# Kernel tuning notes

Measured on AMD Instinct MI355X. Metric: run time of the kernel, lower is better.

## Reference

```python
import jax, jax.numpy as jnp
import numpy as np

N_NODES = 1_000_000
N_EDGES = 16_000_000


def setup_inputs() -> dict:
    key = jax.random.key(0)
    ks = jax.random.split(key, 8)
    x = jax.random.normal(ks[0], (N_NODES, 9), dtype=jnp.float32)
    edge_index = jax.random.randint(ks[1], (2, N_EDGES), 0, N_NODES, dtype=jnp.int64)
    # Glorot-ish scaled params
    W1 = jax.random.normal(ks[2], (9, 16), dtype=jnp.float32) * 0.3
    b1 = jax.random.normal(ks[3], (16,), dtype=jnp.float32) * 0.01
    W2 = jax.random.normal(ks[4], (16, 10), dtype=jnp.float32) * 0.25
    b2 = jax.random.normal(ks[5], (10,), dtype=jnp.float32) * 0.01
    Wf = jax.random.normal(ks[6], (10, 1), dtype=jnp.float32) * 0.3
    bf = jax.random.normal(ks[7], (1,), dtype=jnp.float32) * 0.01
    return {"x": x, "edge_index": edge_index, "W1": W1, "b1": b1,
            "W2": W2, "b2": b2, "Wf": Wf, "bf": bf}


def _gcn_conv(x, W, b, row, col, norm, n):
    # PyG GCNConv: linear transform, then normalized scatter-add aggregation.
    h = x @ W                                   # [N, out]
    msg = h[row] * norm[:, None]                # gather + edgewise scale [E+N, out]
    out = jax.ops.segment_sum(msg, col, num_segments=n)  # scatter-add [N, out]
    return out + b


def reference(x, edge_index, W1, b1, W2, b2, Wf, bf):
    n = x.shape[0]
    # add self-loops (PyG default add_self_loops=True)
    loop = jnp.arange(n, dtype=edge_index.dtype)
    row = jnp.concatenate([edge_index[0], loop])
    col = jnp.concatenate([edge_index[1], loop])
    # symmetric normalization: deg computed over target nodes, weight 1 per edge
    deg = jax.ops.segment_sum(jnp.ones(row.shape[0], dtype=x.dtype), col,
                              num_segments=n)
    deg_inv_sqrt = jnp.where(deg > 0, jax.lax.rsqrt(jnp.maximum(deg, 1.0)), 0.0)
    norm = deg_inv_sqrt[row] * deg_inv_sqrt[col]  # [E+N]

    h = _gcn_conv(x, W1, b1, row, col, norm, n)
    h = jax.nn.relu(h)
    # dropout is identity in eval mode
    h = _gcn_conv(h, W2, b2, row, col, norm, n)
    return h @ Wf + bf
```

## Files before the change

kernel.cpp:

```cpp
#include <hip/hip_runtime.h>

static constexpr int NN = 1000000;
static constexpr int NE = 16000000;
static constexpr int BSH = 11;
static constexpr int BNODES = 1 << BSH;
static constexpr int BMASK = BNODES - 1;
static constexpr int NB = (NN + BMASK) >> BSH;
static constexpr int NWG = 512;
static constexpr int EPW = NE / NWG;


__global__ void k_count(const int* __restrict__ col, int* __restrict__ counts) {
    __shared__ int cnt[NB];
    for (int i = threadIdx.x; i < NB; i += blockDim.x) cnt[i] = 0;
    __syncthreads();
    long long e0 = (long long)blockIdx.x * EPW;
    long long e1 = e0 + EPW; if (e1 > NE) e1 = NE;
    long long e = e0 + threadIdx.x;
    for (; e + 768 < e1; e += 1024) {
        int c0 = col[e], c1 = col[e + 256], c2 = col[e + 512], c3 = col[e + 768];
        atomicAdd(&cnt[c0 >> BSH], 1);
        atomicAdd(&cnt[c1 >> BSH], 1);
        atomicAdd(&cnt[c2 >> BSH], 1);
        atomicAdd(&cnt[c3 >> BSH], 1);
    }
    for (; e < e1; e += 256) atomicAdd(&cnt[col[e] >> BSH], 1);
    __syncthreads();
    int w = blockIdx.x;
    for (int i = threadIdx.x; i < NB; i += blockDim.x)
        counts[i * NWG + w] = cnt[i];
}


__global__ void k_scan_wg(int* __restrict__ counts, int* __restrict__ bucketTotal) {
    __shared__ int sm[NWG];
    int b = blockIdx.x, t = threadIdx.x;
    int v = counts[b * NWG + t];
    sm[t] = v;
    __syncthreads();
    for (int off = 1; off < NWG; off <<= 1) {
        int x = (t >= off) ? sm[t - off] : 0;
        __syncthreads();
        sm[t] += x;
        __syncthreads();
    }
    counts[b * NWG + t] = sm[t] - v;
    if (t == NWG - 1) bucketTotal[b] = sm[t];
}


__global__ void k_scan_total(const int* __restrict__ bucketTotal,
                             int* __restrict__ bucketBase, int* __restrict__ ptr) {
    __shared__ int sm[512];
    int t = threadIdx.x;
    int v = (t < NB) ? bucketTotal[t] : 0;
    sm[t] = v;
    __syncthreads();
    for (int off = 1; off < 512; off <<= 1) {
        int x = (t >= off) ? sm[t - off] : 0;
        __syncthreads();
        sm[t] += x;
        __syncthreads();
    }
    if (t < NB) bucketBase[t] = sm[t] - v;
    if (t == 0) { bucketBase[NB] = NE; ptr[NN] = NE; }
}


__global__ void k_bin2(const int* __restrict__ row, const int* __restrict__ col,
                       const int* __restrict__ counts, const int* __restrict__ bucketBase,
                       unsigned* __restrict__ binned) {
    __shared__ int off[NB];
    int w = blockIdx.x;
    for (int i = threadIdx.x; i < NB; i += blockDim.x)
        off[i] = bucketBase[i] + counts[i * NWG + w];
    __syncthreads();
    long long e0 = (long long)w * EPW;
    long long e1 = e0 + EPW; if (e1 > NE) e1 = NE;
    long long e = e0 + threadIdx.x;
    for (; e + 768 < e1; e += 1024) {
        int c0 = col[e],       r0 = row[e];
        int c1 = col[e + 256], r1 = row[e + 256];
        int c2 = col[e + 512], r2 = row[e + 512];
        int c3 = col[e + 768], r3 = row[e + 768];
        int p0 = atomicAdd(&off[c0 >> BSH], 1);
        int p1 = atomicAdd(&off[c1 >> BSH], 1);
        int p2 = atomicAdd(&off[c2 >> BSH], 1);
        int p3 = atomicAdd(&off[c3 >> BSH], 1);
        binned[p0] = ((unsigned)r0 << BSH) | (unsigned)(c0 & BMASK);
        binned[p1] = ((unsigned)r1 << BSH) | (unsigned)(c1 & BMASK);
        binned[p2] = ((unsigned)r2 << BSH) | (unsigned)(c2 & BMASK);
        binned[p3] = ((unsigned)r3 << BSH) | (unsigned)(c3 & BMASK);
    }
    for (; e < e1; e += 256) {
        int c = col[e], r = row[e];
        int p = atomicAdd(&off[c >> BSH], 1);
        binned[p] = ((unsigned)r << BSH) | (unsigned)(c & BMASK);
    }
}


__global__ __launch_bounds__(512) void k_ptr_dis(const unsigned* __restrict__ binned,
                                                 const int* __restrict__ bucketBase,
                                                 int* __restrict__ ptr,
                                                 float* __restrict__ dis) {
    __shared__ int cnt[BNODES];
    __shared__ int tsum[512];
    int b = blockIdx.x, t = threadIdx.x;
    for (int i = t; i < BNODES; i += 512) cnt[i] = 0;
    __syncthreads();
    int i0 = bucketBase[b], i1 = bucketBase[b + 1];
    int i = i0 + t;
    for (; i + 1536 < i1; i += 2048) {
        unsigned v0 = binned[i],        v1 = binned[i + 512];
        unsigned v2 = binned[i + 1024], v3 = binned[i + 1536];
        atomicAdd(&cnt[v0 & BMASK], 1);
        atomicAdd(&cnt[v1 & BMASK], 1);
        atomicAdd(&cnt[v2 & BMASK], 1);
        atomicAdd(&cnt[v3 & BMASK], 1);
    }
    for (; i < i1; i += 512) atomicAdd(&cnt[binned[i] & BMASK], 1);
    __syncthreads();
    int s0 = cnt[t * 4], s1 = cnt[t * 4 + 1], s2 = cnt[t * 4 + 2], s3 = cnt[t * 4 + 3];
    int tot = s0 + s1 + s2 + s3;
    tsum[t] = tot;
    __syncthreads();
    for (int off = 1; off < 512; off <<= 1) {
        int x = (t >= off) ? tsum[t - off] : 0;
        __syncthreads();
        tsum[t] += x;
        __syncthreads();
    }
    int base = bucketBase[b] + tsum[t] - tot;
    int n0 = (b << BSH) + t * 4;
    if (n0 < NN)     { ptr[n0]     = base;               dis[n0]     = rsqrtf((float)(s0 + 1)); }
    if (n0 + 1 < NN) { ptr[n0 + 1] = base + s0;          dis[n0 + 1] = rsqrtf((float)(s1 + 1)); }
    if (n0 + 2 < NN) { ptr[n0 + 2] = base + s0 + s1;     dis[n0 + 2] = rsqrtf((float)(s2 + 1)); }
    if (n0 + 3 < NN) { ptr[n0 + 3] = base + s0 + s1 + s2; dis[n0 + 3] = rsqrtf((float)(s3 + 1)); }
}


__global__ void k_bucket_scatter(const unsigned* __restrict__ binned,
                                 const int* __restrict__ bucketBase,
                                 const int* __restrict__ ptr,
                                 int* __restrict__ sortedRow) {
    __shared__ int cur[BNODES];
    int b = blockIdx.x;
    int nodeBase = b << BSH;
    for (int i = threadIdx.x; i < BNODES; i += blockDim.x) {
        int n = nodeBase + i;
        cur[i] = (n < NN) ? ptr[n] : 0;
    }
    __syncthreads();
    int i0 = bucketBase[b], i1 = bucketBase[b + 1];
    int i = i0 + threadIdx.x;
    for (; i + 768 < i1; i += 1024) {
        unsigned v0 = binned[i],       v1 = binned[i + 256];
        unsigned v2 = binned[i + 512], v3 = binned[i + 768];
        int p0 = atomicAdd(&cur[v0 & BMASK], 1);
        int p1 = atomicAdd(&cur[v1 & BMASK], 1);
        int p2 = atomicAdd(&cur[v2 & BMASK], 1);
        int p3 = atomicAdd(&cur[v3 & BMASK], 1);
        sortedRow[p0] = (int)(v0 >> BSH);
        sortedRow[p1] = (int)(v1 >> BSH);
        sortedRow[p2] = (int)(v2 >> BSH);
        sortedRow[p3] = (int)(v3 >> BSH);
    }
    for (; i < i1; i += 256) {
        unsigned v = binned[i];
        int pos = atomicAdd(&cur[v & BMASK], 1);
        sortedRow[pos] = (int)(v >> BSH);
    }
}


__global__ void k_lin1(const float* __restrict__ x, const float* __restrict__ W1,
                       const float* __restrict__ dis, float* __restrict__ g1) {
    __shared__ float w[144];
    if (threadIdx.x < 144) w[threadIdx.x] = W1[threadIdx.x];
    __syncthreads();
    int i = blockIdx.x * blockDim.x + threadIdx.x;
    if (i >= NN) return;
    float xv[9];
#pragma unroll
    for (int k = 0; k < 9; ++k) xv[k] = x[(long long)i * 9 + k];
    float d = dis[i];
#pragma unroll
    for (int j = 0; j < 16; ++j) {
        float acc = 0.f;
#pragma unroll
        for (int k = 0; k < 9; ++k) acc = fmaf(xv[k], w[k * 16 + j], acc);
        g1[(long long)i * 16 + j] = acc * d;
    }
}


template <int MODE>
__global__ void k_pull_f(const int* __restrict__ ptr, const int* __restrict__ sortedRow,
                         const float* __restrict__ dis, const float* __restrict__ g,
                         const float* __restrict__ p0, const float* __restrict__ p1,
                         const float* __restrict__ p2, float* __restrict__ dst) {
    __shared__ float w2s[256];
    __shared__ float c16[16];
    __shared__ float wf16[16];
    __shared__ float bfs;
    if (MODE == 0) {
        if (threadIdx.x < 256) {
            int k = threadIdx.x >> 4, j = threadIdx.x & 15;
            w2s[threadIdx.x] = (j < 10) ? p1[k * 10 + j] : 0.f;
        }
        if (threadIdx.x < 16) c16[threadIdx.x] = p0[threadIdx.x];
    } else {
        if (threadIdx.x < 16) {
            c16[threadIdx.x]  = (threadIdx.x < 10) ? p0[threadIdx.x] : 0.f;
            wf16[threadIdx.x] = (threadIdx.x < 10) ? p1[threadIdx.x] : 0.f;
        }
        if (threadIdx.x == 0) bfs = p2[0];
    }
    __syncthreads();

    int grp = threadIdx.x >> 4;
    int j = threadIdx.x & 15;
    int n = blockIdx.x * 16 + grp;
    if (n >= NN) return;
    int e0 = ptr[n], e1 = ptr[n + 1];
    float acc = g[(long long)n * 16 + j];
    int e = e0;
    for (; e + 16 <= e1; e += 16) {
        int r[16];
#pragma unroll
        for (int k = 0; k < 16; ++k) r[k] = sortedRow[e + k];
        float v[16];
#pragma unroll
        for (int k = 0; k < 16; ++k) v[k] = g[(long long)r[k] * 16 + j];
        float s0 = ((v[0] + v[1]) + (v[2] + v[3])) + ((v[4] + v[5]) + (v[6] + v[7]));
        float s1 = ((v[8] + v[9]) + (v[10] + v[11])) + ((v[12] + v[13]) + (v[14] + v[15]));
        acc += s0 + s1;
    }
    for (; e + 4 <= e1; e += 4) {
        int r0 = sortedRow[e + 0], r1 = sortedRow[e + 1];
        int r2 = sortedRow[e + 2], r3 = sortedRow[e + 3];
        float v0 = g[(long long)r0 * 16 + j];
        float v1 = g[(long long)r1 * 16 + j];
        float v2 = g[(long long)r2 * 16 + j];
        float v3 = g[(long long)r3 * 16 + j];
        acc += (v0 + v1) + (v2 + v3);
    }
    for (; e < e1; ++e)
        acc += g[(long long)sortedRow[e] * 16 + j];

    float d = dis[n];
    float val = d * acc;
    if (MODE == 0) {
        float hv = fmaxf(val + c16[j], 0.f);
        float o = 0.f;
#pragma unroll
        for (int k = 0; k < 16; ++k)
            o = fmaf(__shfl(hv, k, 16), w2s[k * 16 + j], o);
        dst[(long long)n * 16 + j] = o * d;
    } else {
        float t = (val + c16[j]) * wf16[j];
#pragma unroll
        for (int m = 8; m >= 1; m >>= 1) t += __shfl_xor(t, m, 16);
        if (j == 0) dst[n] = t + bfs;
    }
}

extern "C" void kernel_launch(void* const* d_in, const int* in_sizes, int n_in,
                              void* d_out, int out_size, void* d_ws, size_t ws_size,
                              hipStream_t stream) {
    const float* x  = (const float*)d_in[0];
    const int*   ei = (const int*)d_in[1];
    const float* W1 = (const float*)d_in[2];
    const float* b1 = (const float*)d_in[3];
    const float* W2 = (const float*)d_in[4];
    const float* b2 = (const float*)d_in[5];
    const float* Wf = (const float*)d_in[6];
    const float* bf = (const float*)d_in[7];
    float* out = (float*)d_out;

    const int* row = ei;
    const int* col = ei + NE;

    char* ws = (char*)d_ws;
    size_t off = 0;
    auto alloc = [&](size_t bytes) -> void* {
        void* p = ws + off;
        off += (bytes + 255) & ~255ULL;
        return p;
    };
    int* counts      = (int*)alloc((size_t)NB * NWG * 4);
    int* bucketTotal = (int*)alloc((size_t)NB * 4);
    int* bucketBase  = (int*)alloc((size_t)(NB + 1) * 4);
    int* ptr         = (int*)alloc((size_t)(NN + 1) * 4);
    float* dis       = (float*)alloc((size_t)NN * 4);
    unsigned* binned = (unsigned*)alloc((size_t)NE * 4);
    int* sortedRow   = (int*)alloc((size_t)NE * 4);
    float* g1        = (float*)alloc((size_t)NN * 16 * 4);

    float* g2 = (float*)binned;

    const int TB = 256;
    const int nodeGrid = (NN + TB - 1) / TB;
    const int pullGrid = (NN + 15) / 16;

    k_count<<<NWG, TB, 0, stream>>>(col, counts);
    k_scan_wg<<<NB, NWG, 0, stream>>>(counts, bucketTotal);
    k_scan_total<<<1, 512, 0, stream>>>(bucketTotal, bucketBase, ptr);
    k_bin2<<<NWG, TB, 0, stream>>>(row, col, counts, bucketBase, binned);
    k_ptr_dis<<<NB, 512, 0, stream>>>(binned, bucketBase, ptr, dis);
    k_bucket_scatter<<<NB, TB, 0, stream>>>(binned, bucketBase, ptr, sortedRow);

    k_lin1<<<nodeGrid, TB, 0, stream>>>(x, W1, dis, g1);
    k_pull_f<0><<<pullGrid, TB, 0, stream>>>(ptr, sortedRow, dis, g1, b1, W2, nullptr, g2);
    k_pull_f<1><<<pullGrid, TB, 0, stream>>>(ptr, sortedRow, dis, g2, b2, Wf, bf, out);
}
```

Baseline: 1.060 ms.

## Stage binned edges in LDS for coalesced writes; fuse ptr/dis with bucket scatter

The bucket binning kernel now stages packed edges per bucket in shared memory and flushes them in contiguous 16-element chunks. This replaces scattered single-word global writes with short contiguous runs, and entries that overflow the staging capacity fall back to direct atomic writes. The degree/ptr kernel is fused with the per-bucket scatter, so the binned array is read twice within one launch and the ptr reload is removed. The costs are large shared-memory use (about 47KB per block), extra barriers each tile, and serial per-bucket flush loops.

```diff
diff --git a/kernel.cpp b/kernel.cpp
--- a/kernel.cpp
+++ b/kernel.cpp
@@ -8,6 +8,9 @@
 static constexpr int NB = (NN + BMASK) >> BSH;
 static constexpr int NWG = 512;
 static constexpr int EPW = NE / NWG;
+static constexpr int CHUNK = 16;
+static constexpr int CAP = 24;
+static constexpr int KE = 4;
 
 
 __global__ void k_count(const int* __restrict__ col, int* __restrict__ counts) {
@@ -67,43 +70,74 @@
 }
 
 
-__global__ void k_bin2(const int* __restrict__ row, const int* __restrict__ col,
-                       const int* __restrict__ counts, const int* __restrict__ bucketBase,
-                       unsigned* __restrict__ binned) {
-    __shared__ int off[NB];
+__global__ __launch_bounds__(256) void k_bin2(const int* __restrict__ row,
+                                              const int* __restrict__ col,
+                                              const int* __restrict__ counts,
+                                              const int* __restrict__ bucketBase,
+                                              unsigned* __restrict__ binned) {
+    __shared__ unsigned stage[NB][CAP];
+    __shared__ int scnt[NB];
+    __shared__ int gcur[NB];
     int w = blockIdx.x;
-    for (int i = threadIdx.x; i < NB; i += blockDim.x)
-        off[i] = bucketBase[i] + counts[i * NWG + w];
+    for (int i = threadIdx.x; i < NB; i += 256) {
+        scnt[i] = 0;
+        gcur[i] = bucketBase[i] + counts[i * NWG + w];
+    }
     __syncthreads();
     long long e0 = (long long)w * EPW;
     long long e1 = e0 + EPW; if (e1 > NE) e1 = NE;
-    long long e = e0 + threadIdx.x;
-    for (; e + 768 < e1; e += 1024) {
-        int c0 = col[e],       r0 = row[e];
-        int c1 = col[e + 256], r1 = row[e + 256];
-        int c2 = col[e + 512], r2 = row[e + 512];
-        int c3 = col[e + 768], r3 = row[e + 768];
-        int p0 = atomicAdd(&off[c0 >> BSH], 1);
-        int p1 = atomicAdd(&off[c1 >> BSH], 1);
-        int p2 = atomicAdd(&off[c2 >> BSH], 1);
-        int p3 = atomicAdd(&off[c3 >> BSH], 1);
-        binned[p0] = ((unsigned)r0 << BSH) | (unsigned)(c0 & BMASK);
-        binned[p1] = ((unsigned)r1 << BSH) | (unsigned)(c1 & BMASK);
-        binned[p2] = ((unsigned)r2 << BSH) | (unsigned)(c2 & BMASK);
-        binned[p3] = ((unsigned)r3 << BSH) | (unsigned)(c3 & BMASK);
-    }
-    for (; e < e1; e += 256) {
-        int c = col[e], r = row[e];
-        int p = atomicAdd(&off[c >> BSH], 1);
-        binned[p] = ((unsigned)r << BSH) | (unsigned)(c & BMASK);
-    }
-}
-
-
-__global__ __launch_bounds__(512) void k_ptr_dis(const unsigned* __restrict__ binned,
-                                                 const int* __restrict__ bucketBase,
-                                                 int* __restrict__ ptr,
-                                                 float* __restrict__ dis) {
+    const int TILE = 256 * KE;
+    for (long long t0 = e0; t0 < e1; t0 += TILE) {
+        int cs[KE], rs[KE];
+        bool ok[KE];
+#pragma unroll
+        for (int k = 0; k < KE; ++k) {
+            long long e = t0 + k * 256 + threadIdx.x;
+            ok[k] = (e < e1);
+            cs[k] = ok[k] ? col[e] : 0;
+            rs[k] = ok[k] ? row[e] : 0;
+        }
+#pragma unroll
+        for (int k = 0; k < KE; ++k) {
+            if (ok[k]) {
+                int b = cs[k] >> BSH;
+                unsigned v = ((unsigned)rs[k] << BSH) | (unsigned)(cs[k] & BMASK);
+                int s = atomicAdd(&scnt[b], 1);
+                if (s < CAP) stage[b][s] = v;
+                else { int p = atomicAdd(&gcur[b], 1); binned[p] = v; }
+            }
+        }
+        __syncthreads();
+        for (int b = threadIdx.x; b < NB; b += 256) {
+            int n = scnt[b]; if (n > CAP) n = CAP;
+            if (n >= CHUNK) {
+                int p = atomicAdd(&gcur[b], CHUNK);
+#pragma unroll
+                for (int q = 0; q < CHUNK; ++q) binned[p + q] = stage[b][q];
+                int rem = n - CHUNK;
+                for (int q = 0; q < rem; ++q) stage[b][q] = stage[b][CHUNK + q];
+                scnt[b] = rem;
+            } else {
+                scnt[b] = n;
+            }
+        }
+        __syncthreads();
+    }
+    for (int b = threadIdx.x; b < NB; b += 256) {
+        int n = scnt[b]; if (n > CAP) n = CAP;
+        if (n > 0) {
+            int p = atomicAdd(&gcur[b], n);
+            for (int q = 0; q < n; ++q) binned[p + q] = stage[b][q];
+        }
+    }
+}
+
+
+__global__ __launch_bounds__(512) void k_sort(const unsigned* __restrict__ binned,
+                                              const int* __restrict__ bucketBase,
+                                              int* __restrict__ ptr,
+                                              float* __restrict__ dis,
+                                              int* __restrict__ sortedRow) {
     __shared__ int cnt[BNODES];
     __shared__ int tsum[512];
     int b = blockIdx.x, t = threadIdx.x;
@@ -133,42 +167,32 @@
     }
     int base = bucketBase[b] + tsum[t] - tot;
     int n0 = (b << BSH) + t * 4;
-    if (n0 < NN)     { ptr[n0]     = base;               dis[n0]     = rsqrtf((float)(s0 + 1)); }
-    if (n0 + 1 < NN) { ptr[n0 + 1] = base + s0;          dis[n0 + 1] = rsqrtf((float)(s1 + 1)); }
-    if (n0 + 2 < NN) { ptr[n0 + 2] = base + s0 + s1;     dis[n0 + 2] = rsqrtf((float)(s2 + 1)); }
+    if (n0 < NN)     { ptr[n0]     = base;                dis[n0]     = rsqrtf((float)(s0 + 1)); }
+    if (n0 + 1 < NN) { ptr[n0 + 1] = base + s0;           dis[n0 + 1] = rsqrtf((float)(s1 + 1)); }
+    if (n0 + 2 < NN) { ptr[n0 + 2] = base + s0 + s1;      dis[n0 + 2] = rsqrtf((float)(s2 + 1)); }
     if (n0 + 3 < NN) { ptr[n0 + 3] = base + s0 + s1 + s2; dis[n0 + 3] = rsqrtf((float)(s3 + 1)); }
-}
-
-
-__global__ void k_bucket_scatter(const unsigned* __restrict__ binned,
-                                 const int* __restrict__ bucketBase,
-                                 const int* __restrict__ ptr,
-                                 int* __restrict__ sortedRow) {
-    __shared__ int cur[BNODES];
-    int b = blockIdx.x;
-    int nodeBase = b << BSH;
-    for (int i = threadIdx.x; i < BNODES; i += blockDim.x) {
-        int n = nodeBase + i;
-        cur[i] = (n < NN) ? ptr[n] : 0;
-    }
-    __syncthreads();
-    int i0 = bucketBase[b], i1 = bucketBase[b + 1];
-    int i = i0 + threadIdx.x;
-    for (; i + 768 < i1; i += 1024) {
-        unsigned v0 = binned[i],       v1 = binned[i + 256];
-        unsigned v2 = binned[i + 512], v3 = binned[i + 768];
-        int p0 = atomicAdd(&cur[v0 & BMASK], 1);
-        int p1 = atomicAdd(&cur[v1 & BMASK], 1);
-        int p2 = atomicAdd(&cur[v2 & BMASK], 1);
-        int p3 = atomicAdd(&cur[v3 & BMASK], 1);
+    __syncthreads();
+    cnt[t * 4]     = base;
+    cnt[t * 4 + 1] = base + s0;
+    cnt[t * 4 + 2] = base + s0 + s1;
+    cnt[t * 4 + 3] = base + s0 + s1 + s2;
+    __syncthreads();
+    i = i0 + t;
+    for (; i + 1536 < i1; i += 2048) {
+        unsigned v0 = binned[i],        v1 = binned[i + 512];
+        unsigned v2 = binned[i + 1024], v3 = binned[i + 1536];
+        int p0 = atomicAdd(&cnt[v0 & BMASK], 1);
+        int p1 = atomicAdd(&cnt[v1 & BMASK], 1);
+        int p2 = atomicAdd(&cnt[v2 & BMASK], 1);
+        int p3 = atomicAdd(&cnt[v3 & BMASK], 1);
         sortedRow[p0] = (int)(v0 >> BSH);
         sortedRow[p1] = (int)(v1 >> BSH);
         sortedRow[p2] = (int)(v2 >> BSH);
         sortedRow[p3] = (int)(v3 >> BSH);
     }
-    for (; i < i1; i += 256) {
+    for (; i < i1; i += 512) {
         unsigned v = binned[i];
-        int pos = atomicAdd(&cur[v & BMASK], 1);
+        int pos = atomicAdd(&cnt[v & BMASK], 1);
         sortedRow[pos] = (int)(v >> BSH);
     }
 }
@@ -308,8 +332,7 @@
     k_scan_wg<<<NB, NWG, 0, stream>>>(counts, bucketTotal);
     k_scan_total<<<1, 512, 0, stream>>>(bucketTotal, bucketBase, ptr);
     k_bin2<<<NWG, TB, 0, stream>>>(row, col, counts, bucketBase, binned);
-    k_ptr_dis<<<NB, 512, 0, stream>>>(binned, bucketBase, ptr, dis);
-    k_bucket_scatter<<<NB, TB, 0, stream>>>(binned, bucketBase, ptr, sortedRow);
+    k_sort<<<NB, 512, 0, stream>>>(binned, bucketBase, ptr, dis, sortedRow);
 
     k_lin1<<<nodeGrid, TB, 0, stream>>>(x, W1, dis, g1);
     k_pull_f<0><<<pullGrid, TB, 0, stream>>>(ptr, sortedRow, dis, g1, b1, W2, nullptr, g2);
```

New measurement: 953.0 us. -10.1%, faster.
